# Performance work log

Hardware: AMD Instinct MI355X
Metric: run time of the kernel (lower is better)

The kernel has to match this reference:

```python
import jax, jax.numpy as jnp
import numpy as np

S, D, F = 4096, 1024, 4096
EPS = 1e-5

def _layernorm(x, g, b):
    mu = jnp.mean(x, axis=-1, keepdims=True)
    var = jnp.mean(jnp.square(x - mu), axis=-1, keepdims=True)
    return (x - mu) * jax.lax.rsqrt(var + EPS) * g + b

def setup_inputs() -> dict:
    key = jax.random.key(0)
    ks = jax.random.split(key, 16)
    s = 0.02
    inp = {
        "query": jax.random.normal(ks[0], (S, D), jnp.float32),
        "key":   jax.random.normal(ks[1], (S, D), jnp.float32),
        "value": jax.random.normal(ks[2], (S, D), jnp.float32),
        "mask":  jax.random.uniform(ks[3], (S, S), jnp.float32),
        # attention linears (stored [in, out]; y = x @ W + b)
        "Wq": jax.random.normal(ks[4], (D, D), jnp.float32) * s,
        "bq": jnp.zeros((D,), jnp.float32),
        "Wk": jax.random.normal(ks[5], (D, D), jnp.float32) * s,
        "bk": jnp.zeros((D,), jnp.float32),
        "Wv": jax.random.normal(ks[6], (D, D), jnp.float32) * s,
        "bv": jnp.zeros((D,), jnp.float32),
        "Wo": jax.random.normal(ks[7], (D, D), jnp.float32) * s,
        "bo": jnp.zeros((D,), jnp.float32),
        # layernorm 1
        "g1": jnp.ones((D,), jnp.float32),
        "be1": jnp.zeros((D,), jnp.float32),
        # feed forward
        "W1": jax.random.normal(ks[8], (D, F), jnp.float32) * s,
        "bf1": jnp.zeros((F,), jnp.float32),
        "W2": jax.random.normal(ks[9], (F, D), jnp.float32) * s,
        "bf2": jnp.zeros((D,), jnp.float32),
        # layernorm 2
        "g2": jnp.ones((D,), jnp.float32),
        "be2": jnp.zeros((D,), jnp.float32),
    }
    return inp

def reference(query, key, value, mask, Wq, bq, Wk, bk, Wv, bv, Wo, bo,
              g1, be1, W1, bf1, W2, bf2, g2, be2):
    q = query @ Wq + bq                      # [S, D]
    k = key @ Wk + bk                        # [S, D]
    v = value @ Wv + bv                      # [S, D]
    scores = q @ k.T                         # [S, S]
    masked = scores * mask                   # multiplicative mask
    h = jax.nn.softmax(masked / jnp.sqrt(jnp.float32(D)), axis=0)  # softmax over dim 0
    attn = (h @ v) @ Wo + bo                 # [S, D]
    # dropout is identity in eval mode
    n1 = _layernorm(attn + query, g1, be1)
    ff = jax.nn.relu(n1 @ W1 + bf1) @ W2 + bf2
    return _layernorm(ff + n1, g2, be2)
```

## Files before the change

### kernel.cpp

```cpp
#include <hip/hip_runtime.h>
#include <hip/hip_bf16.h>

#define S_DIM 4096
#define D_DIM 1024
#define F_DIM 4096

typedef unsigned short ushort_t;
typedef __attribute__((ext_vector_type(8))) short sh8;
typedef __attribute__((ext_vector_type(4))) short sh4;
typedef __attribute__((ext_vector_type(4))) float fx4;

__device__ __forceinline__ ushort_t f2bf(float f) {
    union { float f; unsigned u; } v; v.f = f;
    unsigned r = v.u + 0x7fffu + ((v.u >> 16) & 1u);
    return (ushort_t)(r >> 16);
}
__device__ __forceinline__ float bf2f(ushort_t u) {
    union { unsigned u; float f; } v; v.u = ((unsigned)u) << 16;
    return v.f;
}

typedef const __attribute__((address_space(1))) void* gvp;
typedef __attribute__((address_space(3))) void* svp;
__device__ __forceinline__ void gload_lds16(const void* g, void* l) {
    __builtin_amdgcn_global_load_lds((gvp)g, (svp)l, 16, 0, 0);
}


#define BM 128
#define BN 128
#define BK 32
#define LDS_BUF 16384

template<bool BIAS, bool RELU, bool SCALE, bool OUTBF, bool SPLITK>
__device__ __forceinline__
void gemm_body(const ushort_t* A, const ushort_t* Bt,
               const float* bias,
               float* Cf, ushort_t* Cb,
               int M, int N, int K, int kBeg, int kEnd, float scale)
{
    __shared__ ushort_t lds[3 * (BM * BK + BN * BK)];
    const int tid = threadIdx.x;
    const int bm = blockIdx.x, bn = blockIdx.y;
    const int w  = tid >> 6, l = tid & 63;
    const int wm = w >> 1, wn = w & 1;

    fx4 acc[4][4] = {};

    const ushort_t* Ag = A  + (size_t)(bm * BM) * K;
    const ushort_t* Bg = Bt + (size_t)(bn * BN) * K;

    const int srow = tid >> 2;
    const int scs  = (tid & 3) ^ ((tid >> 3) & 3);

    auto stage = [&](int b, int k0) {
        char* base = (char*)lds + b * LDS_BUF;
        #pragma unroll
        for (int c = 0; c < 2; ++c) {
            int row = c * 64 + srow;
            gload_lds16(Ag + (size_t)row * K + k0 + scs * 8,
                        base + c * 4096 + tid * 16);
            gload_lds16(Bg + (size_t)row * K + k0 + scs * 8,
                        base + 8192 + c * 4096 + tid * 16);
        }
    };

    const int nt = (kEnd - kBeg) / BK;

    stage(0, kBeg);
    if (nt > 1) {
        stage(1, kBeg + BK);
        asm volatile("s_waitcnt vmcnt(4)" ::: "memory");
    } else {
        asm volatile("s_waitcnt vmcnt(0)" ::: "memory");
    }
    __builtin_amdgcn_s_barrier();
    __builtin_amdgcn_sched_barrier(0);

    const int rchunk = (l >> 4) ^ ((l >> 1) & 3);

    int cur = 0;
    for (int t = 0; t < nt; ++t) {
        int stg = cur + 2; if (stg >= 3) stg -= 3;
        if (t + 2 < nt) stage(stg, kBeg + (t + 2) * BK);

        char* lbase = (char*)lds + cur * LDS_BUF;
        sh8 af[4], bfr[4];
        #pragma unroll
        for (int q = 0; q < 4; ++q) {
            int ra = wm * 64 + q * 16 + (l & 15);
            af[q]  = *(const sh8*)(lbase + ra * 64 + rchunk * 16);
            int rb = wn * 64 + q * 16 + (l & 15);
            bfr[q] = *(const sh8*)(lbase + 8192 + rb * 64 + rchunk * 16);
        }
        #pragma unroll
        for (int i = 0; i < 4; ++i)
            #pragma unroll
            for (int j = 0; j < 4; ++j)
                acc[i][j] = __builtin_amdgcn_mfma_f32_16x16x32_bf16(
                                af[i], bfr[j], acc[i][j], 0, 0, 0);

        asm volatile("s_waitcnt lgkmcnt(0)" ::: "memory");
        if (t + 2 < nt)      asm volatile("s_waitcnt vmcnt(4)" ::: "memory");
        else if (t + 1 < nt) asm volatile("s_waitcnt vmcnt(0)" ::: "memory");
        if (t + 1 < nt) {
            __builtin_amdgcn_s_barrier();
            __builtin_amdgcn_sched_barrier(0);
        }
        cur = cur + 1; if (cur == 3) cur = 0;
    }

    if (SPLITK) Cb += (size_t)blockIdx.z * M * N;

    const int crow0 = bm * BM + wm * 64;
    const int ccol0 = bn * BN + wn * 64;
    #pragma unroll
    for (int i = 0; i < 4; ++i) {
        #pragma unroll
        for (int j = 0; j < 4; ++j) {
            int col = ccol0 + j * 16 + (l & 15);
            float bia = BIAS ? bias[col] : 0.f;
            #pragma unroll
            for (int r = 0; r < 4; ++r) {
                int row = crow0 + i * 16 + (l >> 4) * 4 + r;
                float v = acc[i][j][r] + bia;
                if (SCALE) v *= scale;
                if (RELU) v = fmaxf(v, 0.f);
                if (OUTBF) Cb[(size_t)row * N + col] = f2bf(v);
                else       Cf[(size_t)row * N + col] = v;
            }
        }
    }
}

template<bool BIAS, bool RELU, bool SCALE, bool OUTBF>
__global__ __launch_bounds__(256)
void gemm_bt(const ushort_t* __restrict__ A, const ushort_t* __restrict__ Bt,
             const float* __restrict__ bias,
             float* __restrict__ Cf, ushort_t* __restrict__ Cb,
             int M, int N, int K, float scale)
{
    gemm_body<BIAS, RELU, SCALE, OUTBF, false>(A, Bt, bias, Cf, Cb,
                                               M, N, K, 0, K, scale);
}

__global__ __launch_bounds__(256)
void gemm_bt_sk(const ushort_t* __restrict__ A, const ushort_t* __restrict__ Bt,
                ushort_t* __restrict__ Cpart, int M, int N, int K, int Ks)
{
    int z = blockIdx.z;
    gemm_body<false, false, false, true, true>(A, Bt, nullptr,
                                               nullptr, Cpart,
                                               M, N, K, z * Ks, z * Ks + Ks, 1.f);
}

__global__ __launch_bounds__(256)
void qkv_gemm(const ushort_t* qin, const ushort_t* kin, const ushort_t* vin,
              const ushort_t* WqT, const ushort_t* WkT, const ushort_t* WvT,
              const float* bq, const float* bk, const float* bv,
              ushort_t* qb, ushort_t* kb, ushort_t* vb, int M, int N, int K)
{
    const ushort_t* A; const ushort_t* Bt; const float* bias; ushort_t* C;
    if (blockIdx.z == 0)      { A = qin; Bt = WqT; bias = bq; C = qb; }
    else if (blockIdx.z == 1) { A = kin; Bt = WkT; bias = bk; C = kb; }
    else                      { A = vin; Bt = WvT; bias = bv; C = vb; }
    gemm_body<true, false, false, true, false>(A, Bt, bias,
                                               nullptr, C, M, N, K, 0, K, 1.f);
}

#define G2_BM 256
#define G2_BN 256
#define G2_BUF 32768

template<bool BIAS, bool RELU, bool SCALE, bool MASKMUL, bool OUTBF, bool SPLITK>
__device__ __forceinline__
void gemm256_body(const ushort_t* A, const ushort_t* Bt,
                  const float* bias, const float* mask,
                  float* Cf, ushort_t* Cb,
                  int M, int N, int K, int kBeg, int kEnd, float scale)
{
    __shared__ ushort_t lds[3 * (G2_BM * BK + G2_BN * BK)];
    const int tid = threadIdx.x;
    const int bm = blockIdx.x, bn = blockIdx.y;
    const int w  = tid >> 6, l = tid & 63;
    const int wm = w >> 2, wn = w & 3;

    fx4 acc[8][4] = {};

    const ushort_t* Ag = A  + (size_t)(bm * G2_BM) * K;
    const ushort_t* Bg = Bt + (size_t)(bn * G2_BN) * K;

    const int scs = (tid & 3) ^ ((tid >> 3) & 3);

    auto stage = [&](int b, int k0) {
        char* base = (char*)lds + b * G2_BUF;
        #pragma unroll
        for (int c = 0; c < 2; ++c) {
            int idx = c * 512 + tid;
            int row = idx >> 2;
            gload_lds16(Ag + (size_t)row * K + k0 + scs * 8,
                        base + idx * 16);
            gload_lds16(Bg + (size_t)row * K + k0 + scs * 8,
                        base + 16384 + idx * 16);
        }
    };

    const int nt = (kEnd - kBeg) / BK;

    stage(0, kBeg);
    if (nt > 1) {
        stage(1, kBeg + BK);
        asm volatile("s_waitcnt vmcnt(4)" ::: "memory");
    } else {
        asm volatile("s_waitcnt vmcnt(0)" ::: "memory");
    }
    __builtin_amdgcn_s_barrier();
    __builtin_amdgcn_sched_barrier(0);

    const int rchunk = (l >> 4) ^ ((l >> 1) & 3);

    int cur = 0;
    for (int t = 0; t < nt; ++t) {
        int stg = cur + 2; if (stg >= 3) stg -= 3;
        if (t + 2 < nt) stage(stg, kBeg + (t + 2) * BK);

        char* lbase = (char*)lds + cur * G2_BUF;
        sh8 af[8], bfr[4];
        #pragma unroll
        for (int q = 0; q < 8; ++q) {
            int ra = wm * 128 + q * 16 + (l & 15);
            af[q] = *(const sh8*)(lbase + ra * 64 + rchunk * 16);
        }
        #pragma unroll
        for (int j = 0; j < 4; ++j) {
            int rb = wn * 64 + j * 16 + (l & 15);
            bfr[j] = *(const sh8*)(lbase + 16384 + rb * 64 + rchunk * 16);
        }
        #pragma unroll
        for (int i = 0; i < 8; ++i)
            #pragma unroll
            for (int j = 0; j < 4; ++j)
                acc[i][j] = __builtin_amdgcn_mfma_f32_16x16x32_bf16(
                                af[i], bfr[j], acc[i][j], 0, 0, 0);

        asm volatile("s_waitcnt lgkmcnt(0)" ::: "memory");
        if (t + 2 < nt)      asm volatile("s_waitcnt vmcnt(4)" ::: "memory");
        else if (t + 1 < nt) asm volatile("s_waitcnt vmcnt(0)" ::: "memory");
        if (t + 1 < nt) {
            __builtin_amdgcn_s_barrier();
            __builtin_amdgcn_sched_barrier(0);
        }
        cur = cur + 1; if (cur == 3) cur = 0;
    }

    if (SPLITK) Cb += (size_t)blockIdx.z * M * N;

    const int crow0 = bm * G2_BM + wm * 128;
    const int ccol0 = bn * G2_BN + wn * 64;
    #pragma unroll
    for (int i = 0; i < 8; ++i) {
        #pragma unroll
        for (int j = 0; j < 4; ++j) {
            int col = ccol0 + j * 16 + (l & 15);
            float bia = BIAS ? bias[col] : 0.f;
            #pragma unroll
            for (int r = 0; r < 4; ++r) {
                int row = crow0 + i * 16 + (l >> 4) * 4 + r;
                float v = acc[i][j][r] + bia;
                if (SCALE) v *= scale;
                if (MASKMUL) v *= mask[(size_t)row * N + col];
                if (RELU) v = fmaxf(v, 0.f);
                if (OUTBF) Cb[(size_t)row * N + col] = f2bf(v);
                else       Cf[(size_t)row * N + col] = v;
            }
        }
    }
}

template<bool BIAS, bool RELU, bool SCALE, bool MASKMUL, bool OUTBF>
__global__ __launch_bounds__(512)
void gemm256_bt(const ushort_t* __restrict__ A, const ushort_t* __restrict__ Bt,
                const float* __restrict__ bias, const float* __restrict__ mask,
                float* __restrict__ Cf, ushort_t* __restrict__ Cb,
                int M, int N, int K, float scale)
{
    gemm256_body<BIAS, RELU, SCALE, MASKMUL, OUTBF, false>(
        A, Bt, bias, mask, Cf, Cb, M, N, K, 0, K, scale);
}

__global__ __launch_bounds__(512)
void gemm256_bt_sk(const ushort_t* __restrict__ A, const ushort_t* __restrict__ Bt,
                   ushort_t* __restrict__ Cpart, int M, int N, int K, int Ks)
{
    int z = blockIdx.z;
    gemm256_body<false, false, false, false, true, true>(
        A, Bt, nullptr, nullptr, nullptr, Cpart,
        M, N, K, z * Ks, z * Ks + Ks, 1.f);
}

template<int NS>
__global__ __launch_bounds__(256)
void reduce_sk(const ushort_t* __restrict__ parts, ushort_t* __restrict__ ob,
               size_t MN)
{
    size_t idx = ((size_t)blockIdx.x * 256 + threadIdx.x) * 8;
    float s[8] = {0.f, 0.f, 0.f, 0.f, 0.f, 0.f, 0.f, 0.f};
    #pragma unroll
    for (int p = 0; p < NS; ++p) {
        sh8 v = *(const sh8*)(parts + (size_t)p * MN + idx);
        #pragma unroll
        for (int j = 0; j < 8; ++j) s[j] += bf2f((ushort_t)v[j]);
    }
    sh8 r;
    #pragma unroll
    for (int j = 0; j < 8; ++j) r[j] = (short)f2bf(s[j]);
    *(sh8*)(ob + idx) = r;
}

__global__ __launch_bounds__(256)
void transpose_f32_bf16(const float* __restrict__ in, ushort_t* __restrict__ out,
                        int R, int C)
{
    __shared__ float t[32][33];
    int bc = blockIdx.x * 32, br = blockIdx.y * 32;
    int tx = threadIdx.x & 31, ty = threadIdx.x >> 5;
    #pragma unroll
    for (int i = 0; i < 32; i += 8)
        t[ty + i][tx] = in[(size_t)(br + ty + i) * C + bc + tx];
    __syncthreads();
    #pragma unroll
    for (int i = 0; i < 32; i += 8)
        out[(size_t)(bc + ty + i) * R + br + tx] = f2bf(t[tx][ty + i]);
}

__global__ __launch_bounds__(256)
void transpose4_f32_bf16(const float* w0, const float* w1,
                         const float* w2, const float* w3,
                         ushort_t* o0, ushort_t* o1, ushort_t* o2, ushort_t* o3)
{
    const int R = D_DIM, C = D_DIM;
    const float* in; ushort_t* out;
    if (blockIdx.z == 0)      { in = w0; out = o0; }
    else if (blockIdx.z == 1) { in = w1; out = o1; }
    else if (blockIdx.z == 2) { in = w2; out = o2; }
    else                      { in = w3; out = o3; }
    __shared__ float t[32][33];
    int bc = blockIdx.x * 32, br = blockIdx.y * 32;
    int tx = threadIdx.x & 31, ty = threadIdx.x >> 5;
    #pragma unroll
    for (int i = 0; i < 32; i += 8)
        t[ty + i][tx] = in[(size_t)(br + ty + i) * C + bc + tx];
    __syncthreads();
    #pragma unroll
    for (int i = 0; i < 32; i += 8)
        out[(size_t)(bc + ty + i) * R + br + tx] = f2bf(t[tx][ty + i]);
}

__global__ __launch_bounds__(256)
void transpose_bf16(const ushort_t* __restrict__ in, ushort_t* __restrict__ out,
                    int R, int C)
{
    __shared__ ushort_t t[32][33];
    int bc = blockIdx.x * 32, br = blockIdx.y * 32;
    int tx = threadIdx.x & 31, ty = threadIdx.x >> 5;
    #pragma unroll
    for (int i = 0; i < 32; i += 8)
        t[ty + i][tx] = in[(size_t)(br + ty + i) * C + bc + tx];
    __syncthreads();
    #pragma unroll
    for (int i = 0; i < 32; i += 8)
        out[(size_t)(bc + ty + i) * R + br + tx] = t[tx][ty + i];
}

__global__ __launch_bounds__(256)
void cvt_bf16_3(const float* a, const float* b, const float* c,
                ushort_t* oa, ushort_t* ob, ushort_t* oc)
{
    const float* in; ushort_t* out;
    if (blockIdx.y == 0)      { in = a; out = oa; }
    else if (blockIdx.y == 1) { in = b; out = ob; }
    else                      { in = c; out = oc; }
    int i = (blockIdx.x * 256 + threadIdx.x) * 8;
    const float4* p = (const float4*)(in + i);
    float4 x = p[0], y = p[1];
    sh8 r;
    r[0] = (short)f2bf(x.x); r[1] = (short)f2bf(x.y);
    r[2] = (short)f2bf(x.z); r[3] = (short)f2bf(x.w);
    r[4] = (short)f2bf(y.x); r[5] = (short)f2bf(y.y);
    r[6] = (short)f2bf(y.z); r[7] = (short)f2bf(y.w);
    *(sh8*)(out + i) = r;
}

#define NCH 256
#define ROWS_PER_CH (S_DIM / NCH)

__global__ __launch_bounds__(256)
void smax_pass1(const ushort_t* __restrict__ m,
                float* __restrict__ pmax, float* __restrict__ psum)
{
    int c0 = (blockIdx.x * 256 + threadIdx.x) * 8;
    int chunk = blockIdx.y;
    int r0 = chunk * ROWS_PER_CH;

    float mx[8], sm[8];
    #pragma unroll
    for (int j = 0; j < 8; ++j) { mx[j] = -1e30f; sm[j] = 0.f; }

    for (int i = 0; i < ROWS_PER_CH; ++i) {
        size_t off = (size_t)(r0 + i) * S_DIM + c0;
        sh8 mv = *(const sh8*)(m + off);
        #pragma unroll
        for (int j = 0; j < 8; ++j) {
            float v = bf2f((ushort_t)mv[j]);
            float nm = fmaxf(mx[j], v);
            sm[j] = sm[j] * __expf(mx[j] - nm) + __expf(v - nm);
            mx[j] = nm;
        }
    }
    #pragma unroll
    for (int j = 0; j < 8; ++j) {
        pmax[(size_t)chunk * S_DIM + c0 + j] = mx[j];
        psum[(size_t)chunk * S_DIM + c0 + j] = sm[j];
    }
}

__global__ __launch_bounds__(256)
void smax_pass2(const float* __restrict__ pmax, const float* __restrict__ psum,
                float* __restrict__ cmax, float* __restrict__ cinv)
{
    int col = blockIdx.x * 256 + threadIdx.x;
    float mx = -1e30f, sm = 0.f;
    for (int c = 0; c < NCH; ++c) {
        float m2 = pmax[(size_t)c * S_DIM + col];
        float s2 = psum[(size_t)c * S_DIM + col];
        float nm = fmaxf(mx, m2);
        sm = sm * __expf(mx - nm) + s2 * __expf(m2 - nm);
        mx = nm;
    }
    cmax[col] = mx;
    cinv[col] = 1.f / sm;
}

__global__ __launch_bounds__(256)
void smax_pass3(const ushort_t* __restrict__ m,
                const float* __restrict__ cmax, const float* __restrict__ cinv,
                ushort_t* __restrict__ h)
{
    size_t idx = ((size_t)blockIdx.x * 256 + threadIdx.x) * 8;
    int col0 = (int)(idx & (S_DIM - 1));
    sh8 mv = *(const sh8*)(m + idx);
    sh8 r;
    #pragma unroll
    for (int j = 0; j < 8; ++j) {
        int c = col0 + j;
        float v = bf2f((ushort_t)mv[j]);
        r[j] = (short)f2bf(__expf(v - cmax[c]) * cinv[c]);
    }
    *(sh8*)(h + idx) = r;
}

template<int NS, bool WB>
__global__ __launch_bounds__(256)
void add_ln_sk(const ushort_t* __restrict__ parts, const float* __restrict__ pbias,
               const float* __restrict__ resid, const float* __restrict__ g,
               const float* __restrict__ be,
               float* __restrict__ of, ushort_t* __restrict__ ob)
{
    const int D = D_DIM;
    const size_t SD = (size_t)S_DIM * D_DIM;
    int row = blockIdx.x, tid = threadIdx.x;
    size_t base = (size_t)row * D + tid * 4;

    float4 vr = *(const float4*)(resid + base);
    float4 vbi = ((const float4*)pbias)[tid];
    float x0 = vr.x + vbi.x, x1 = vr.y + vbi.y, x2 = vr.z + vbi.z, x3 = vr.w + vbi.w;
    #pragma unroll
    for (int p = 0; p < NS; ++p) {
        sh4 v = *(const sh4*)(parts + p * SD + base);
        x0 += bf2f((ushort_t)v[0]); x1 += bf2f((ushort_t)v[1]);
        x2 += bf2f((ushort_t)v[2]); x3 += bf2f((ushort_t)v[3]);
    }

    float s = x0 + x1 + x2 + x3;
    float q = x0 * x0 + x1 * x1 + x2 * x2 + x3 * x3;
    #pragma unroll
    for (int off = 32; off; off >>= 1) {
        s += __shfl_down(s, off);
        q += __shfl_down(q, off);
    }
    __shared__ float red[8];
    int w = tid >> 6, l = tid & 63;
    if (!l) { red[w] = s; red[4 + w] = q; }
    __syncthreads();
    s = red[0] + red[1] + red[2] + red[3];
    q = red[4] + red[5] + red[6] + red[7];
    float mu = s * (1.f / D);
    float rstd = rsqrtf(q * (1.f / D) - mu * mu + 1e-5f);
    float4 vg  = ((const float4*)g)[tid];
    float4 vbe = ((const float4*)be)[tid];
    float y0 = (x0 - mu) * rstd * vg.x + vbe.x;
    float y1 = (x1 - mu) * rstd * vg.y + vbe.y;
    float y2 = (x2 - mu) * rstd * vg.z + vbe.z;
    float y3 = (x3 - mu) * rstd * vg.w + vbe.w;
    float4 r; r.x = y0; r.y = y1; r.z = y2; r.w = y3;
    *(float4*)(of + base) = r;
    if (WB) {
        sh4 rb;
        rb[0] = (short)f2bf(y0); rb[1] = (short)f2bf(y1);
        rb[2] = (short)f2bf(y2); rb[3] = (short)f2bf(y3);
        *(sh4*)(ob + base) = rb;
    }
}

extern "C" void kernel_launch(void* const* d_in, const int* in_sizes, int n_in,
                              void* d_out, int out_size, void* d_ws, size_t ws_size,
                              hipStream_t stream)
{
    const float* query = (const float*)d_in[0];
    const float* key_  = (const float*)d_in[1];
    const float* value = (const float*)d_in[2];
    const float* mask  = (const float*)d_in[3];
    const float* Wq = (const float*)d_in[4];  const float* bq = (const float*)d_in[5];
    const float* Wk = (const float*)d_in[6];  const float* bk = (const float*)d_in[7];
    const float* Wv = (const float*)d_in[8];  const float* bv = (const float*)d_in[9];
    const float* Wo = (const float*)d_in[10]; const float* bo = (const float*)d_in[11];
    const float* g1 = (const float*)d_in[12]; const float* be1 = (const float*)d_in[13];
    const float* W1 = (const float*)d_in[14]; const float* bf1 = (const float*)d_in[15];
    const float* W2 = (const float*)d_in[16]; const float* bf2 = (const float*)d_in[17];
    const float* g2 = (const float*)d_in[18]; const float* be2 = (const float*)d_in[19];

    const size_t MB = 1ull << 20;
    char* ws = (char*)d_ws;
    ushort_t* WqT = (ushort_t*)(ws);
    ushort_t* WkT = (ushort_t*)(ws + 2 * MB);
    ushort_t* WvT = (ushort_t*)(ws + 4 * MB);
    ushort_t* WoT = (ushort_t*)(ws + 6 * MB);
    ushort_t* W1T = (ushort_t*)(ws + 8 * MB);
    ushort_t* W2T = (ushort_t*)(ws + 16 * MB);
    ushort_t* qin = (ushort_t*)(ws + 24 * MB);
    ushort_t* kin = (ushort_t*)(ws + 32 * MB);
    ushort_t* vin = (ushort_t*)(ws + 40 * MB);
    ushort_t* qb  = (ushort_t*)(ws + 48 * MB);
    ushort_t* kb  = (ushort_t*)(ws + 56 * MB);
    ushort_t* vb  = (ushort_t*)(ws + 64 * MB);
    ushort_t* vT  = (ushort_t*)(ws + 72 * MB);
    ushort_t* msc = (ushort_t*)(ws + 80 * MB);
    ushort_t* hb  = (ushort_t*)(ws + 112 * MB);
    float*   pmax = (float*)(ws + 144 * MB);
    float*   psum = (float*)(ws + 148 * MB);
    float*   cmax = (float*)(ws + 152 * MB);
    float*   cinv = (float*)(ws + 152 * MB + 64 * 1024);
    ushort_t* pts1  = (ushort_t*)(ws + 80 * MB);
    ushort_t* apb   = (ushort_t*)(ws + 24 * MB);
    ushort_t* pts2  = (ushort_t*)(ws + 80 * MB);
    float*    n1f   = (float*)(ws + 48 * MB);
    ushort_t* n1b   = (ushort_t*)(ws + 64 * MB);
    ushort_t* mid   = (ushort_t*)(ws + 112 * MB);
    ushort_t* pts3  = (ushort_t*)(ws + 80 * MB);

    const int S = S_DIM, D = D_DIM, F = F_DIM;

    transpose4_f32_bf16<<<dim3(D / 32, D / 32, 4), 256, 0, stream>>>(
        Wq, Wk, Wv, Wo, WqT, WkT, WvT, WoT);
    transpose_f32_bf16<<<dim3(F / 32, D / 32), 256, 0, stream>>>(W1, W1T, D, F);
    transpose_f32_bf16<<<dim3(D / 32, F / 32), 256, 0, stream>>>(W2, W2T, F, D);

    cvt_bf16_3<<<dim3(S * D / 8 / 256, 3), 256, 0, stream>>>(
        query, key_, value, qin, kin, vin);

    qkv_gemm<<<dim3(S / BM, D / BN, 3), 256, 0, stream>>>(
        qin, kin, vin, WqT, WkT, WvT, bq, bk, bv, qb, kb, vb, S, D, D);

    transpose_bf16<<<dim3(D / 32, S / 32), 256, 0, stream>>>(vb, vT, S, D);

    gemm256_bt<false, false, true, true, true>
        <<<dim3(S / G2_BM, S / G2_BN), 512, 0, stream>>>(
        qb, kb, nullptr, mask, nullptr, msc, S, S, D, 0.03125f);

    smax_pass1<<<dim3(S / 2048, NCH), 256, 0, stream>>>(msc, pmax, psum);
    smax_pass2<<<S / 256, 256, 0, stream>>>(pmax, psum, cmax, cinv);
    smax_pass3<<<(size_t)S * S / 8 / 256, 256, 0, stream>>>(msc, cmax, cinv, hb);

    gemm256_bt_sk<<<dim3(S / G2_BM, D / G2_BN, 4), 512, 0, stream>>>(
        hb, vT, pts1, S, D, S, S / 4);
    reduce_sk<4><<<S * D / 2048, 256, 0, stream>>>(pts1, apb, (size_t)S * D);

    gemm_bt_sk<<<dim3(S / BM, D / BN, 2), 256, 0, stream>>>(apb, WoT, pts2, S, D, D, D / 2);

    add_ln_sk<2, true><<<S, 256, 0, stream>>>(pts2, bo, query, g1, be1, n1f, n1b);

    gemm256_bt<true, true, false, false, true>
        <<<dim3(S / G2_BM, F / G2_BN), 512, 0, stream>>>(
        n1b, W1T, bf1, nullptr, nullptr, mid, S, F, D, 1.f);

    gemm256_bt_sk<<<dim3(S / G2_BM, D / G2_BN, 4), 512, 0, stream>>>(
        mid, W2T, pts3, S, D, F, F / 4);

    add_ln_sk<4, false><<<S, 256, 0, stream>>>(pts3, bf2, n1f, g2, be2,
                                               (float*)d_out, nullptr);
}
```

Measured before the change: 332.9 us.

## Interleave LDS reads, global prefetch and MFMA in four phases per K-tile

```diff
diff --git a/kernel.cpp b/kernel.cpp
--- a/kernel.cpp
+++ b/kernel.cpp
@@ -192,24 +192,24 @@
 
     const int scs = (tid & 3) ^ ((tid >> 3) & 3);
 
-    auto stage = [&](int b, int k0) {
+    auto stage_q = [&](int b, int k0, int p) {
         char* base = (char*)lds + b * G2_BUF;
-        #pragma unroll
-        for (int c = 0; c < 2; ++c) {
-            int idx = c * 512 + tid;
-            int row = idx >> 2;
-            gload_lds16(Ag + (size_t)row * K + k0 + scs * 8,
-                        base + idx * 16);
+        int idx = (p & 1) * 512 + tid;
+        int row = idx >> 2;
+        if (p < 2)
+            gload_lds16(Ag + (size_t)row * K + k0 + scs * 8, base + idx * 16);
+        else
             gload_lds16(Bg + (size_t)row * K + k0 + scs * 8,
                         base + 16384 + idx * 16);
-        }
     };
 
     const int nt = (kEnd - kBeg) / BK;
 
-    stage(0, kBeg);
+    #pragma unroll
+    for (int p = 0; p < 4; ++p) stage_q(0, kBeg, p);
     if (nt > 1) {
-        stage(1, kBeg + BK);
+        #pragma unroll
+        for (int p = 0; p < 4; ++p) stage_q(1, kBeg + BK, p);
         asm volatile("s_waitcnt vmcnt(4)" ::: "memory");
     } else {
         asm volatile("s_waitcnt vmcnt(0)" ::: "memory");
@@ -222,33 +222,43 @@
     int cur = 0;
     for (int t = 0; t < nt; ++t) {
         int stg = cur + 2; if (stg >= 3) stg -= 3;
-        if (t + 2 < nt) stage(stg, kBeg + (t + 2) * BK);
-
         char* lbase = (char*)lds + cur * G2_BUF;
-        sh8 af[8], bfr[4];
-        #pragma unroll
-        for (int q = 0; q < 8; ++q) {
-            int ra = wm * 128 + q * 16 + (l & 15);
-            af[q] = *(const sh8*)(lbase + ra * 64 + rchunk * 16);
-        }
-        #pragma unroll
-        for (int j = 0; j < 4; ++j) {
-            int rb = wn * 64 + j * 16 + (l & 15);
-            bfr[j] = *(const sh8*)(lbase + 16384 + rb * 64 + rchunk * 16);
-        }
-        #pragma unroll
-        for (int i = 0; i < 8; ++i)
+
+        sh8 bfr[4];
+        #pragma unroll
+        for (int p = 0; p < 4; ++p) {
+            int ra0 = wm * 128 + (2 * p) * 16 + (l & 15);
+            sh8 a0 = *(const sh8*)(lbase + ra0 * 64 + rchunk * 16);
+            sh8 a1 = *(const sh8*)(lbase + (ra0 + 16) * 64 + rchunk * 16);
+            if (p == 0) {
+                #pragma unroll
+                for (int j = 0; j < 4; ++j) {
+                    int rb = wn * 64 + j * 16 + (l & 15);
+                    bfr[j] = *(const sh8*)(lbase + 16384 + rb * 64 + rchunk * 16);
+                }
+            }
+            if (t + 2 < nt) stage_q(stg, kBeg + (t + 2) * BK, p);
+
+            __builtin_amdgcn_s_barrier();
+            asm volatile("s_waitcnt lgkmcnt(0)" ::: "memory");
+            __builtin_amdgcn_sched_barrier(0);
+            __builtin_amdgcn_s_setprio(1);
             #pragma unroll
-            for (int j = 0; j < 4; ++j)
-                acc[i][j] = __builtin_amdgcn_mfma_f32_16x16x32_bf16(
-                                af[i], bfr[j], acc[i][j], 0, 0, 0);
-
-        asm volatile("s_waitcnt lgkmcnt(0)" ::: "memory");
-        if (t + 2 < nt)      asm volatile("s_waitcnt vmcnt(4)" ::: "memory");
-        else if (t + 1 < nt) asm volatile("s_waitcnt vmcnt(0)" ::: "memory");
-        if (t + 1 < nt) {
-            __builtin_amdgcn_s_barrier();
-            __builtin_amdgcn_sched_barrier(0);
+            for (int j = 0; j < 4; ++j) {
+                acc[2 * p][j] = __builtin_amdgcn_mfma_f32_16x16x32_bf16(
+                                    a0, bfr[j], acc[2 * p][j], 0, 0, 0);
+                acc[2 * p + 1][j] = __builtin_amdgcn_mfma_f32_16x16x32_bf16(
+                                    a1, bfr[j], acc[2 * p + 1][j], 0, 0, 0);
+            }
+            __builtin_amdgcn_s_setprio(0);
+            if (p == 3) {
+                if (t + 2 < nt)      asm volatile("s_waitcnt vmcnt(4)" ::: "memory");
+                else if (t + 1 < nt) asm volatile("s_waitcnt vmcnt(0)" ::: "memory");
+            }
+            if (p < 3 || t + 1 < nt) {
+                __builtin_amdgcn_s_barrier();
+                __builtin_amdgcn_sched_barrier(0);
+            }
         }
         cur = cur + 1; if (cur == 3) cur = 0;
     }
```

Result: no change. 335.8 us (+0.9%).

## Rewrite 256x256 GEMM as BK=64 double-buffered ping-pong pipeline with interleaved staging

Applied to the files above, without the earlier changes.

```diff
diff --git a/kernel.cpp b/kernel.cpp
--- a/kernel.cpp
+++ b/kernel.cpp
@@ -25,7 +25,6 @@
 __device__ __forceinline__ void gload_lds16(const void* g, void* l) {
     __builtin_amdgcn_global_load_lds((gvp)g, (svp)l, 16, 0, 0);
 }
-
 
 #define BM 128
 #define BN 128
@@ -168,18 +167,18 @@
                                                nullptr, C, M, N, K, 0, K, 1.f);
 }
 
-#define G2_BM 256
-#define G2_BN 256
-#define G2_BUF 32768
+#define P_BM 256
+#define P_BN 256
+#define P_BK 64
 
 template<bool BIAS, bool RELU, bool SCALE, bool MASKMUL, bool OUTBF, bool SPLITK>
 __device__ __forceinline__
-void gemm256_body(const ushort_t* A, const ushort_t* Bt,
-                  const float* bias, const float* mask,
-                  float* Cf, ushort_t* Cb,
-                  int M, int N, int K, int kBeg, int kEnd, float scale)
-{
-    __shared__ ushort_t lds[3 * (G2_BM * BK + G2_BN * BK)];
+void gemm8p_body(const ushort_t* A, const ushort_t* Bt,
+                 const float* bias, const float* mask,
+                 float* Cf, ushort_t* Cb,
+                 int M, int N, int K, int kBeg, int kEnd, float scale)
+{
+    extern __shared__ char plds[];
     const int tid = threadIdx.x;
     const int bm = blockIdx.x, bn = blockIdx.y;
     const int w  = tid >> 6, l = tid & 63;
@@ -187,29 +186,40 @@
 
     fx4 acc[8][4] = {};
 
-    const ushort_t* Ag = A  + (size_t)(bm * G2_BM) * K;
-    const ushort_t* Bg = Bt + (size_t)(bn * G2_BN) * K;
-
-    const int scs = (tid & 3) ^ ((tid >> 3) & 3);
-
-    auto stage = [&](int b, int k0) {
-        char* base = (char*)lds + b * G2_BUF;
+    const ushort_t* Ag = A  + (size_t)(bm * P_BM) * K;
+    const ushort_t* Bg = Bt + (size_t)(bn * P_BN) * K;
+
+    const int s_lc = (tid & 7) ^ ((tid >> 3) & 7);
+
+    auto stageH = [&](int t, int op, int h) {
+        int k0 = kBeg + t * P_BK;
+        char* base = plds + (t & 1) * 65536 + op * 32768 + h * 16384;
+        const ushort_t* G = op ? Bg : Ag;
         #pragma unroll
         for (int c = 0; c < 2; ++c) {
             int idx = c * 512 + tid;
-            int row = idx >> 2;
-            gload_lds16(Ag + (size_t)row * K + k0 + scs * 8,
+            int row = idx >> 3;
+            gload_lds16(G + (size_t)(h * 128 + row) * K + k0 + s_lc * 8,
                         base + idx * 16);
-            gload_lds16(Bg + (size_t)row * K + k0 + scs * 8,
-                        base + 16384 + idx * 16);
         }
     };
 
-    const int nt = (kEnd - kBeg) / BK;
-
-    stage(0, kBeg);
+    auto ldA = [&](int d, int row, int kk) -> sh8 {
+        int half = row >> 7, lr = row & 127;
+        int chp = (kk * 4 + (l >> 4)) ^ (l & 7);
+        return *(const sh8*)(plds + d * 65536 + half * 16384 + lr * 128 + chp * 16);
+    };
+    auto ldB = [&](int d, int row, int kk) -> sh8 {
+        int half = row >> 7, lr = row & 127;
+        int chp = (kk * 4 + (l >> 4)) ^ (l & 7);
+        return *(const sh8*)(plds + d * 65536 + 32768 + half * 16384 + lr * 128 + chp * 16);
+    };
+
+    const int nt = (kEnd - kBeg) / P_BK;
+
+    stageH(0, 0, 0); stageH(0, 0, 1); stageH(0, 1, 0); stageH(0, 1, 1);
     if (nt > 1) {
-        stage(1, kBeg + BK);
+        stageH(1, 1, 0); stageH(1, 1, 1);
         asm volatile("s_waitcnt vmcnt(4)" ::: "memory");
     } else {
         asm volatile("s_waitcnt vmcnt(0)" ::: "memory");
@@ -217,46 +227,63 @@
     __builtin_amdgcn_s_barrier();
     __builtin_amdgcn_sched_barrier(0);
 
-    const int rchunk = (l >> 4) ^ ((l >> 1) & 3);
-
-    int cur = 0;
-    for (int t = 0; t < nt; ++t) {
-        int stg = cur + 2; if (stg >= 3) stg -= 3;
-        if (t + 2 < nt) stage(stg, kBeg + (t + 2) * BK);
-
-        char* lbase = (char*)lds + cur * G2_BUF;
-        sh8 af[8], bfr[4];
-        #pragma unroll
-        for (int q = 0; q < 8; ++q) {
-            int ra = wm * 128 + q * 16 + (l & 15);
-            af[q] = *(const sh8*)(lbase + ra * 64 + rchunk * 16);
-        }
-        #pragma unroll
-        for (int j = 0; j < 4; ++j) {
-            int rb = wn * 64 + j * 16 + (l & 15);
-            bfr[j] = *(const sh8*)(lbase + 16384 + rb * 64 + rchunk * 16);
-        }
-        #pragma unroll
-        for (int i = 0; i < 8; ++i)
+    sh8 bfr[4][2];
+    for (int u = 0; u < nt; u += 2) {
+        #pragma unroll
+        for (int hv = 0; hv < 2; ++hv) {
+            const int t = u + hv;
+            const int d = t & 1;
             #pragma unroll
-            for (int j = 0; j < 4; ++j)
-                acc[i][j] = __builtin_amdgcn_mfma_f32_16x16x32_bf16(
-                                af[i], bfr[j], acc[i][j], 0, 0, 0);
-
-        asm volatile("s_waitcnt lgkmcnt(0)" ::: "memory");
-        if (t + 2 < nt)      asm volatile("s_waitcnt vmcnt(4)" ::: "memory");
-        else if (t + 1 < nt) asm volatile("s_waitcnt vmcnt(0)" ::: "memory");
-        if (t + 1 < nt) {
-            __builtin_amdgcn_s_barrier();
-            __builtin_amdgcn_sched_barrier(0);
-        }
-        cur = cur + 1; if (cur == 3) cur = 0;
+            for (int q = 0; q < 4; ++q) {
+                const int i0 = 2 * q;
+                int ra = wm * 128 + i0 * 16 + (l & 15);
+                sh8 a00 = ldA(d, ra, 0);
+                sh8 a01 = ldA(d, ra, 1);
+                sh8 a10 = ldA(d, ra + 16, 0);
+                sh8 a11 = ldA(d, ra + 16, 1);
+                if (q == 0) {
+                    #pragma unroll
+                    for (int j = 0; j < 4; ++j) {
+                        int rb = wn * 64 + j * 16 + (l & 15);
+                        bfr[j][0] = ldB(d, rb, 0);
+                        bfr[j][1] = ldB(d, rb, 1);
+                    }
+                }
+                if (q == 0)      { if (t + 1 < nt) stageH(t + 1, 0, 0); }
+                else if (q == 1) { if (t + 1 < nt) stageH(t + 1, 0, 1); }
+                else if (q == 2) { if (t + 2 < nt) stageH(t + 2, 1, 0); }
+                else             { if (t + 2 < nt) stageH(t + 2, 1, 1); }
+
+                __builtin_amdgcn_s_barrier();
+                asm volatile("s_waitcnt lgkmcnt(0)" ::: "memory");
+                __builtin_amdgcn_sched_barrier(0);
+                __builtin_amdgcn_s_setprio(1);
+                #pragma unroll
+                for (int j = 0; j < 4; ++j) {
+                    acc[i0][j] = __builtin_amdgcn_mfma_f32_16x16x32_bf16(
+                                     a00, bfr[j][0], acc[i0][j], 0, 0, 0);
+                    acc[i0][j] = __builtin_amdgcn_mfma_f32_16x16x32_bf16(
+                                     a01, bfr[j][1], acc[i0][j], 0, 0, 0);
+                    acc[i0 + 1][j] = __builtin_amdgcn_mfma_f32_16x16x32_bf16(
+                                     a10, bfr[j][0], acc[i0 + 1][j], 0, 0, 0);
+                    acc[i0 + 1][j] = __builtin_amdgcn_mfma_f32_16x16x32_bf16(
+                                     a11, bfr[j][1], acc[i0 + 1][j], 0, 0, 0);
+                }
+                __builtin_amdgcn_s_setprio(0);
+                if (q == 3) {
+                    if (t + 2 < nt)      asm volatile("s_waitcnt vmcnt(4)" ::: "memory");
+                    else if (t + 1 < nt) asm volatile("s_waitcnt vmcnt(0)" ::: "memory");
+                }
+                __builtin_amdgcn_s_barrier();
+                __builtin_amdgcn_sched_barrier(0);
+            }
+        }
     }
 
     if (SPLITK) Cb += (size_t)blockIdx.z * M * N;
 
-    const int crow0 = bm * G2_BM + wm * 128;
-    const int ccol0 = bn * G2_BN + wn * 64;
+    const int crow0 = bm * P_BM + wm * 128;
+    const int ccol0 = bn * P_BN + wn * 64;
     #pragma unroll
     for (int i = 0; i < 8; ++i) {
         #pragma unroll
@@ -278,22 +305,22 @@
 }
 
 template<bool BIAS, bool RELU, bool SCALE, bool MASKMUL, bool OUTBF>
-__global__ __launch_bounds__(512)
-void gemm256_bt(const ushort_t* __restrict__ A, const ushort_t* __restrict__ Bt,
-                const float* __restrict__ bias, const float* __restrict__ mask,
-                float* __restrict__ Cf, ushort_t* __restrict__ Cb,
-                int M, int N, int K, float scale)
-{
-    gemm256_body<BIAS, RELU, SCALE, MASKMUL, OUTBF, false>(
+__global__ __launch_bounds__(512, 1)
+void gemm8p_bt(const ushort_t* __restrict__ A, const ushort_t* __restrict__ Bt,
+               const float* __restrict__ bias, const float* __restrict__ mask,
+               float* __restrict__ Cf, ushort_t* __restrict__ Cb,
+               int M, int N, int K, float scale)
+{
+    gemm8p_body<BIAS, RELU, SCALE, MASKMUL, OUTBF, false>(
         A, Bt, bias, mask, Cf, Cb, M, N, K, 0, K, scale);
 }
 
-__global__ __launch_bounds__(512)
-void gemm256_bt_sk(const ushort_t* __restrict__ A, const ushort_t* __restrict__ Bt,
-                   ushort_t* __restrict__ Cpart, int M, int N, int K, int Ks)
+__global__ __launch_bounds__(512, 1)
+void gemm8p_bt_sk(const ushort_t* __restrict__ A, const ushort_t* __restrict__ Bt,
+                  ushort_t* __restrict__ Cpart, int M, int N, int K, int Ks)
 {
     int z = blockIdx.z;
-    gemm256_body<false, false, false, false, true, true>(
+    gemm8p_body<false, false, false, false, true, true>(
         A, Bt, nullptr, nullptr, nullptr, Cpart,
         M, N, K, z * Ks, z * Ks + Ks, 1.f);
 }
@@ -559,6 +586,7 @@
     ushort_t* pts3  = (ushort_t*)(ws + 80 * MB);
 
     const int S = S_DIM, D = D_DIM, F = F_DIM;
+    const size_t P_LDS = 131072;
 
     transpose4_f32_bf16<<<dim3(D / 32, D / 32, 4), 256, 0, stream>>>(
         Wq, Wk, Wv, Wo, WqT, WkT, WvT, WoT);
@@ -573,15 +601,15 @@
 
     transpose_bf16<<<dim3(D / 32, S / 32), 256, 0, stream>>>(vb, vT, S, D);
 
-    gemm256_bt<false, false, true, true, true>
-        <<<dim3(S / G2_BM, S / G2_BN), 512, 0, stream>>>(
+    gemm8p_bt<false, false, true, true, true>
+        <<<dim3(S / P_BM, S / P_BN), 512, P_LDS, stream>>>(
         qb, kb, nullptr, mask, nullptr, msc, S, S, D, 0.03125f);
 
     smax_pass1<<<dim3(S / 2048, NCH), 256, 0, stream>>>(msc, pmax, psum);
     smax_pass2<<<S / 256, 256, 0, stream>>>(pmax, psum, cmax, cinv);
     smax_pass3<<<(size_t)S * S / 8 / 256, 256, 0, stream>>>(msc, cmax, cinv, hb);
 
-    gemm256_bt_sk<<<dim3(S / G2_BM, D / G2_BN, 4), 512, 0, stream>>>(
+    gemm8p_bt_sk<<<dim3(S / P_BM, D / P_BN, 4), 512, P_LDS, stream>>>(
         hb, vT, pts1, S, D, S, S / 4);
     reduce_sk<4><<<S * D / 2048, 256, 0, stream>>>(pts1, apb, (size_t)S * D);
 
@@ -589,11 +617,11 @@
 
     add_ln_sk<2, true><<<S, 256, 0, stream>>>(pts2, bo, query, g1, be1, n1f, n1b);
 
-    gemm256_bt<true, true, false, false, true>
-        <<<dim3(S / G2_BM, F / G2_BN), 512, 0, stream>>>(
+    gemm8p_bt<true, true, false, false, true>
+        <<<dim3(S / P_BM, F / P_BN), 512, P_LDS, stream>>>(
         n1b, W1T, bf1, nullptr, nullptr, mid, S, F, D, 1.f);
 
-    gemm256_bt_sk<<<dim3(S / G2_BM, D / G2_BN, 4), 512, 0, stream>>>(
+    gemm8p_bt_sk<<<dim3(S / P_BM, D / P_BN, 4), 512, P_LDS, stream>>>(
         mid, W2T, pts3, S, D, F, F / 4);
 
     add_ln_sk<4, false><<<S, 256, 0, stream>>>(pts3, bf2, n1f, g2, be2,
```

After: 331.9 us. Within noise of the previous version (-0.3%).
